# Kernel tuning notes

Hardware: AMD Instinct MI355X
Metric: run time of the kernel (lower is better)

Reference implementation:

```python
import jax, jax.numpy as jnp
import numpy as np

VOCAB = 50257
N = 2048          # neuron_dim
K = int(N * 0.01) # k-WTA winners = 20
LR = 0.01
EPS = 1e-8
T = 128           # sequence length


def setup_inputs() -> dict:
    key = jax.random.key(0)
    k1, k2, k3 = jax.random.split(key, 3)
    tokens = jax.random.randint(k1, (T,), 0, VOCAB)
    # stands in for nn.init.orthogonal_ random projection table [vocab, N]
    projection = jax.random.normal(k2, (VOCAB, N), dtype=jnp.float32)
    # sigma buffer starts at zeros in the module but is seeded by pre_train/seed_backstory;
    # use a clamped random state in [0,1) so the recurrence does real work.
    sigma = jax.random.uniform(k3, (N, N), dtype=jnp.float32)
    return {"tokens": tokens, "projection": projection, "sigma": sigma, "plasticity": 1}


def _sparse_activation(projection, tokens):
    raw = projection[tokens]                      # [T, N] gather
    top_val = jax.lax.top_k(raw, K)[0]            # [T, K]
    thr = top_val[:, -1:]                         # k-th largest value per row
    return (raw >= thr).astype(jnp.float32)       # binary k-WTA codes (ties kept, as in torch)


def reference(tokens, projection, sigma, plasticity):
    acts = _sparse_activation(projection, tokens)  # [T, N]
    x_curr = acts[:-1]                             # [T-1, N]
    x_next = acts[1:]                              # [T-1, N]
    if plasticity:
        sqrt_k = jnp.sqrt(jnp.float32(K))

        def step(sig, xs):
            x, xn = xs
            pred = sig @ x                                   # mv: [N]
            pn = jnp.linalg.norm(pred)
            overlap = jnp.dot(pred, xn) / (pn * sqrt_k + EPS)
            tension = jnp.where(pn > 0, 1.0 - overlap, 1.0)
            # Hebbian outer-product update + clamp to [0,1]
            sig = jnp.clip(sig + LR * jnp.outer(xn, x), 0.0, 1.0)
            return sig, tension

        _, tensions = jax.lax.scan(step, sigma, (x_curr, x_next))
        return tensions                                      # [T-1]
    else:
        preds = x_curr @ sigma.T                             # [T-1, N]
        dot = jnp.sum(preds * x_next, axis=-1)
        overlap = dot / (jnp.linalg.norm(preds, axis=-1) * jnp.linalg.norm(x_next, axis=-1) + EPS)
        return 1.0 - overlap
```

## Files before the change

### kernel.cpp

```cpp
#include <hip/hip_runtime.h>
#include <hip/hip_bf16.h>
#include <math.h>

#define NV    2048
#define TT    128
#define TM1   127
#define KK    20
#define LRC   0.01f
#define EPSC  1e-8f


__global__ __launch_bounds__(256) void act_kernel(
    const int* __restrict__ tokens, const float* __restrict__ proj,
    int* __restrict__ act_idx, int* __restrict__ act_cnt,
    int* __restrict__ occCnt, unsigned char* __restrict__ occList)
{
    const int t    = blockIdx.x;
    const int tid  = threadIdx.x;
    const int lane = tid & 63;
    const int wid  = tid >> 6;

    const float* __restrict__ row = proj + (size_t)tokens[t] * (size_t)NV;

    float v[8];
    #pragma unroll
    for (int r = 0; r < 8; ++r) v[r] = row[r * 256 + tid];

    __shared__ float wmax[4];
    __shared__ float gmaxS;
    __shared__ int   winner;

    float thr = 0.0f;
    for (int it = 0; it < KK; ++it) {
        __syncthreads();
        float lm = v[0];
        #pragma unroll
        for (int r = 1; r < 8; ++r) lm = fmaxf(lm, v[r]);
        #pragma unroll
        for (int off = 32; off; off >>= 1) lm = fmaxf(lm, __shfl_down(lm, off));
        if (lane == 0) wmax[wid] = lm;
        __syncthreads();
        if (tid == 0) {
            gmaxS  = fmaxf(fmaxf(wmax[0], wmax[1]), fmaxf(wmax[2], wmax[3]));
            winner = 0x7fffffff;
        }
        __syncthreads();
        const float gm = gmaxS;
        int cand = 0x7fffffff;
        #pragma unroll
        for (int r = 0; r < 8; ++r)
            if (cand == 0x7fffffff && v[r] == gm) cand = tid * 8 + r;
        if (cand != 0x7fffffff) atomicMin(&winner, cand);
        __syncthreads();
        const int wn = winner;
        if ((wn >> 3) == tid) v[wn & 7] = -__builtin_inff();
        thr = gm;
    }

    __shared__ int idxLDS[64];
    __shared__ int cntS;
    __syncthreads();
    if (wid == 0) {
        int base = 0;
        for (int round = 0; round < NV / 64; ++round) {
            const int i = round * 64 + lane;
            const bool p = (row[i] >= thr);
            const unsigned long long m = __ballot(p);
            const int pos = base + (int)__popcll(m & ((1ull << lane) - 1ull));
            if (p && pos < 64) idxLDS[pos] = i;
            base += (int)__popcll(m);
        }
        if (lane == 0) cntS = base < 64 ? base : 64;
    }
    __syncthreads();
    const int cnt = cntS;
    if (tid == 0) act_cnt[t] = cnt;
    if (tid < cnt) {
        const int j = idxLDS[tid];
        act_idx[t * 64 + tid] = j;
        const int slot = atomicAdd(&occCnt[j], 1);
        occList[j * 128 + slot] = (unsigned char)t;
    }
}

__global__ __launch_bounds__(256) void transpose_kernel(
    const float* __restrict__ in, float* __restrict__ out)
{
    __shared__ float tile[32][33];
    const int tx = threadIdx.x;
    const int ty = threadIdx.y;
    const int x0 = blockIdx.x * 32;
    const int y0 = blockIdx.y * 32;
    #pragma unroll
    for (int k = 0; k < 4; ++k)
        tile[ty + k * 8][tx] = in[(size_t)(y0 + ty + k * 8) * NV + x0 + tx];
    __syncthreads();
    #pragma unroll
    for (int k = 0; k < 4; ++k)
        out[(size_t)(x0 + ty + k * 8) * NV + y0 + tx] = tile[tx][ty + k * 8];
}

__global__ __launch_bounds__(512) void tension_kernel(
    const float* __restrict__ sigma0, const float* __restrict__ ST0,
    const int* __restrict__ act_idx, const int* __restrict__ act_cnt,
    const int* __restrict__ occCnt, const unsigned char* __restrict__ occList,
    const int* __restrict__ plast, float* __restrict__ out)
{
    const int t    = blockIdx.x;
    const int tid  = threadIdx.x;
    const int lane = tid & 63;
    const int wid  = tid >> 6;

    __shared__ float          predS[NV];
    __shared__ float          deltaS[NV];
    __shared__ unsigned int   cnt[NV];
    __shared__ unsigned short list[NV];
    __shared__ unsigned int   listCnt;
    __shared__ int            acur[64], anext[64];
    __shared__ float          wsum[8];

    const int ccur  = act_cnt[t];
    const int cnext = act_cnt[t + 1];
    if (tid < 64) {
        acur[tid]  = act_idx[t * 64 + tid];
        anext[tid] = act_idx[(t + 1) * 64 + tid];
    }
    for (int i = tid; i < NV; i += 512) { deltaS[i] = 0.0f; cnt[i] = 0u; }
    if (tid == 0) listCnt = 0u;
    __syncthreads();

    float acc[4] = {0.f, 0.f, 0.f, 0.f};
    for (int jj = 0; jj < ccur; ++jj) {
        const float* __restrict__ rowp = ST0 + (size_t)acur[jj] * NV;
        #pragma unroll
        for (int r = 0; r < 4; ++r) acc[r] += rowp[r * 512 + tid];
    }

    const bool plas = (plast[0] != 0);
    if (plas) {
        for (int jj = 0; jj < ccur; ++jj) {
            const int j  = acur[jj];
            const int oc = occCnt[j];
            for (int p = tid; p < oc * 64; p += 512) {
                const int o  = p >> 6;
                const int ii = p & 63;
                const int s  = (int)occList[j * 128 + o];
                if (s < t) {
                    const int cs = act_cnt[s + 1];
                    if (ii < cs) {
                        const int i = act_idx[(s + 1) * 64 + ii];
                        const unsigned old = atomicAdd(&cnt[i], 1u);
                        if (old == 0u) {
                            const unsigned pos = atomicAdd(&listCnt, 1u);
                            list[pos] = (unsigned short)i;
                        }
                    }
                }
            }
            __syncthreads();
            const unsigned L = listCnt;
            __syncthreads();
            for (unsigned e = tid; e < L; e += 512) {
                const int i = (int)list[e];
                const unsigned c = cnt[i];
                const float s0 = sigma0[(size_t)i * NV + j];
                deltaS[i] += fminf(1.0f - s0, LRC * (float)c);
                cnt[i] = 0u;
            }
            if (tid == 0) listCnt = 0u;
            __syncthreads();
        }
    }

    #pragma unroll
    for (int r = 0; r < 4; ++r) {
        const int i = r * 512 + tid;
        predS[i] = acc[r] + deltaS[i];
    }
    __syncthreads();

    float loc = 0.0f;
    #pragma unroll
    for (int r = 0; r < 4; ++r) { const float p = predS[r * 512 + tid]; loc += p * p; }
    #pragma unroll
    for (int off = 32; off; off >>= 1) loc += __shfl_down(loc, off);
    if (lane == 0) wsum[wid] = loc;
    __syncthreads();

    if (tid < 64) {
        float n2 = 0.0f;
        #pragma unroll
        for (int w = 0; w < 8; ++w) n2 += wsum[w];
        float d = (tid < cnext) ? predS[anext[tid]] : 0.0f;
        #pragma unroll
        for (int off = 32; off; off >>= 1) d += __shfl_down(d, off);
        if (tid == 0) {
            const float pn = sqrtf(n2);
            float tens;
            if (plas) {
                const float overlap = d / (pn * sqrtf((float)KK) + EPSC);
                tens = (pn > 0.0f) ? (1.0f - overlap) : 1.0f;
            } else {
                const float overlap = d / (pn * sqrtf((float)cnext) + EPSC);
                tens = 1.0f - overlap;
            }
            out[t] = tens;
        }
    }
}

extern "C" void kernel_launch(void* const* d_in, const int* in_sizes, int n_in,
                              void* d_out, int out_size, void* d_ws, size_t ws_size,
                              hipStream_t stream)
{
    const int*   tokens = (const int*)d_in[0];
    const float* proj   = (const float*)d_in[1];
    const float* sigma  = (const float*)d_in[2];
    const int*   plast  = (const int*)d_in[3];
    float*       out    = (float*)d_out;

    char* ws = (char*)d_ws;
    int*           act_idx = (int*)(ws + 0);
    int*           act_cnt = (int*)(ws + 32768);
    int*           occCnt  = (int*)(ws + 33280);
    unsigned char* occList = (unsigned char*)(ws + 41472);
    float*         ST0     = (float*)(ws + 303616);

    hipMemsetAsync(occCnt, 0, NV * sizeof(int), stream);
    act_kernel<<<TT, 256, 0, stream>>>(tokens, proj, act_idx, act_cnt, occCnt, occList);
    transpose_kernel<<<dim3(NV / 32, NV / 32), dim3(32, 8), 0, stream>>>(sigma, ST0);
    tension_kernel<<<TM1, 512, 0, stream>>>(sigma, ST0, act_idx, act_cnt, occCnt,
                                            occList, plast, out);
}
```

Baseline: 503.6 us.

## Batch Hebbian count accumulation across active columns and use per-wave top-k merge

The tension kernel now accumulates co-occurrence counts for up to 20 active columns at once in packed 16-bit shared counters, then has each thread sum its own rows' clipped deltas. This replaces the per-column atomic list building and the two barriers per column. The activation kernel now finds per-wave top-20 candidates with xor shuffles and no block barriers, then merges them on one thread to get the threshold. In exchange it uses a larger shared-memory counter array, which may lower occupancy, and it scans all rows per column instead of only the touched ones.

```diff
diff --git a/kernel.cpp b/kernel.cpp
--- a/kernel.cpp
+++ b/kernel.cpp
@@ -8,6 +8,7 @@
 #define KK    20
 #define LRC   0.01f
 #define EPSC  1e-8f
+#define CHK   20
 
 
 __global__ __launch_bounds__(256) void act_kernel(
@@ -24,51 +25,62 @@
 
     float v[8];
     #pragma unroll
-    for (int r = 0; r < 8; ++r) v[r] = row[r * 256 + tid];
-
-    __shared__ float wmax[4];
-    __shared__ float gmaxS;
-    __shared__ int   winner;
-
-    float thr = 0.0f;
+    for (int r = 0; r < 8; ++r) v[r] = row[wid * 512 + r * 64 + lane];
+
+    __shared__ float wcand[4][KK];
+    __shared__ float thrS;
+    __shared__ int   idxLDS[64];
+    __shared__ int   cntS;
+
     for (int it = 0; it < KK; ++it) {
-        __syncthreads();
         float lm = v[0];
         #pragma unroll
         for (int r = 1; r < 8; ++r) lm = fmaxf(lm, v[r]);
         #pragma unroll
-        for (int off = 32; off; off >>= 1) lm = fmaxf(lm, __shfl_down(lm, off));
-        if (lane == 0) wmax[wid] = lm;
-        __syncthreads();
-        if (tid == 0) {
-            gmaxS  = fmaxf(fmaxf(wmax[0], wmax[1]), fmaxf(wmax[2], wmax[3]));
-            winner = 0x7fffffff;
-        }
-        __syncthreads();
-        const float gm = gmaxS;
-        int cand = 0x7fffffff;
-        #pragma unroll
-        for (int r = 0; r < 8; ++r)
-            if (cand == 0x7fffffff && v[r] == gm) cand = tid * 8 + r;
-        if (cand != 0x7fffffff) atomicMin(&winner, cand);
-        __syncthreads();
-        const int wn = winner;
-        if ((wn >> 3) == tid) v[wn & 7] = -__builtin_inff();
-        thr = gm;
-    }
-
-    __shared__ int idxLDS[64];
-    __shared__ int cntS;
-    __syncthreads();
+        for (int off = 1; off < 64; off <<= 1) lm = fmaxf(lm, __shfl_xor(lm, off));
+        bool has = false;
+        #pragma unroll
+        for (int r = 0; r < 8; ++r) has = has || (v[r] == lm);
+        const unsigned long long m = __ballot(has);
+        if (lane == (int)(__ffsll((long long)m) - 1)) {
+            bool done = false;
+            #pragma unroll
+            for (int r = 0; r < 8; ++r)
+                if (!done && v[r] == lm) { v[r] = -__builtin_inff(); done = true; }
+        }
+        if (lane == 0) wcand[wid][it] = lm;
+    }
+    __syncthreads();
+
+    if (tid == 0) {
+        int p0 = 0, p1 = 0, p2 = 0, p3 = 0;
+        float th = 0.0f;
+        for (int k = 0; k < KK; ++k) {
+            float bv = -__builtin_inff(); int bw = 0;
+            if (p0 < KK && wcand[0][p0] > bv) { bv = wcand[0][p0]; bw = 0; }
+            if (p1 < KK && wcand[1][p1] > bv) { bv = wcand[1][p1]; bw = 1; }
+            if (p2 < KK && wcand[2][p2] > bv) { bv = wcand[2][p2]; bw = 2; }
+            if (p3 < KK && wcand[3][p3] > bv) { bv = wcand[3][p3]; bw = 3; }
+            if      (bw == 0) ++p0;
+            else if (bw == 1) ++p1;
+            else if (bw == 2) ++p2;
+            else              ++p3;
+            th = bv;
+        }
+        thrS = th;
+    }
+    __syncthreads();
+    const float thr = thrS;
+
     if (wid == 0) {
         int base = 0;
         for (int round = 0; round < NV / 64; ++round) {
             const int i = round * 64 + lane;
             const bool p = (row[i] >= thr);
-            const unsigned long long m = __ballot(p);
-            const int pos = base + (int)__popcll(m & ((1ull << lane) - 1ull));
+            const unsigned long long mm = __ballot(p);
+            const int pos = base + (int)__popcll(mm & ((1ull << lane) - 1ull));
             if (p && pos < 64) idxLDS[pos] = i;
-            base += (int)__popcll(m);
+            base += (int)__popcll(mm);
         }
         if (lane == 0) cntS = base < 64 ? base : 64;
     }
@@ -111,13 +123,10 @@
     const int lane = tid & 63;
     const int wid  = tid >> 6;
 
-    __shared__ float          predS[NV];
-    __shared__ float          deltaS[NV];
-    __shared__ unsigned int   cnt[NV];
-    __shared__ unsigned short list[NV];
-    __shared__ unsigned int   listCnt;
-    __shared__ int            acur[64], anext[64];
-    __shared__ float          wsum[8];
+    __shared__ float        predS[NV];
+    __shared__ unsigned int cnt32[CHK * 1024];
+    __shared__ int          acur[64], anext[64];
+    __shared__ float        wsum[8];
 
     const int ccur  = act_cnt[t];
     const int cnext = act_cnt[t + 1];
@@ -125,8 +134,6 @@
         acur[tid]  = act_idx[t * 64 + tid];
         anext[tid] = act_idx[(t + 1) * 64 + tid];
     }
-    for (int i = tid; i < NV; i += 512) { deltaS[i] = 0.0f; cnt[i] = 0u; }
-    if (tid == 0) listCnt = 0u;
     __syncthreads();
 
     float acc[4] = {0.f, 0.f, 0.f, 0.f};
@@ -136,38 +143,48 @@
         for (int r = 0; r < 4; ++r) acc[r] += rowp[r * 512 + tid];
     }
 
+    float dsum[4] = {0.f, 0.f, 0.f, 0.f};
     const bool plas = (plast[0] != 0);
     if (plas) {
-        for (int jj = 0; jj < ccur; ++jj) {
-            const int j  = acur[jj];
-            const int oc = occCnt[j];
-            for (int p = tid; p < oc * 64; p += 512) {
-                const int o  = p >> 6;
-                const int ii = p & 63;
-                const int s  = (int)occList[j * 128 + o];
-                if (s < t) {
-                    const int cs = act_cnt[s + 1];
-                    if (ii < cs) {
-                        const int i = act_idx[(s + 1) * 64 + ii];
-                        const unsigned old = atomicAdd(&cnt[i], 1u);
-                        if (old == 0u) {
-                            const unsigned pos = atomicAdd(&listCnt, 1u);
-                            list[pos] = (unsigned short)i;
+        for (int jc = 0; jc < ccur; jc += CHK) {
+            const int je = (jc + CHK < ccur) ? jc + CHK : ccur;
+            for (int e = tid; e < (je - jc) * 1024; e += 512) cnt32[e] = 0u;
+            __syncthreads();
+
+            for (int jj = jc; jj < je; ++jj) {
+                const int j    = acur[jj];
+                const int oc   = occCnt[j];
+                const int base = (jj - jc) * 1024;
+                for (int p = tid; p < oc * 64; p += 512) {
+                    const int o  = p >> 6;
+                    const int ii = p & 63;
+                    const int s  = (int)occList[j * 128 + o];
+                    if (s < t) {
+                        const int cs = act_cnt[s + 1];
+                        if (ii < cs) {
+                            const int i = act_idx[(s + 1) * 64 + ii];
+                            atomicAdd(&cnt32[base + (i >> 1)],
+                                      (i & 1) ? 65536u : 1u);
                         }
                     }
                 }
             }
             __syncthreads();
-            const unsigned L = listCnt;
-            __syncthreads();
-            for (unsigned e = tid; e < L; e += 512) {
-                const int i = (int)list[e];
-                const unsigned c = cnt[i];
-                const float s0 = sigma0[(size_t)i * NV + j];
-                deltaS[i] += fminf(1.0f - s0, LRC * (float)c);
-                cnt[i] = 0u;
+
+            #pragma unroll
+            for (int r = 0; r < 4; ++r) {
+                const int i = r * 512 + tid;
+                float ds = 0.f;
+                for (int jj = jc; jj < je; ++jj) {
+                    const unsigned w = cnt32[(jj - jc) * 1024 + (i >> 1)];
+                    const unsigned c = (i & 1) ? (w >> 16) : (w & 0xffffu);
+                    if (c) {
+                        const float s0 = sigma0[(size_t)i * NV + acur[jj]];
+                        ds += fminf(1.0f - s0, LRC * (float)c);
+                    }
+                }
+                dsum[r] += ds;
             }
-            if (tid == 0) listCnt = 0u;
             __syncthreads();
         }
     }
@@ -175,7 +192,7 @@
     #pragma unroll
     for (int r = 0; r < 4; ++r) {
         const int i = r * 512 + tid;
-        predS[i] = acc[r] + deltaS[i];
+        predS[i] = acc[r] + dsum[r];
     }
     __syncthreads();
 
```

Result: no change. 510.1 us (+1.3%).
